# Optimization experiments

Measured on AMD Instinct MI355X. Metric: run time of the kernel, lower is better.

Reference implementation:

```python
import jax, jax.numpy as jnp
import numpy as np

B, C, H, W = 8, 256, 56, 56
R = 2
E = C // R  # embed_dim = in_channels // r


def setup_inputs() -> dict:
    key = jax.random.key(0)
    ks = jax.random.split(key, 10)
    s = 0.02
    return {
        "x": jax.random.normal(ks[0], (B, C, H, W), jnp.float32),
        "Wq": jax.random.normal(ks[1], (E, C), jnp.float32) * s,
        "bq": jax.random.normal(ks[2], (E,), jnp.float32) * s,
        "Wk": jax.random.normal(ks[3], (E, C), jnp.float32) * s,
        "bk": jax.random.normal(ks[4], (E,), jnp.float32) * s,
        "Wv": jax.random.normal(ks[5], (E, C), jnp.float32) * s,
        "bv": jax.random.normal(ks[6], (E,), jnp.float32) * s,
        "Wcat": jax.random.normal(ks[7], (1, 2 * E), jnp.float32) * s,  # 1x1 conv, no bias
        "Wexp": jax.random.normal(ks[8], (C, E), jnp.float32) * s,
        "bexp": jax.random.normal(ks[9], (C,), jnp.float32) * s,
    }


def reference(x, Wq, bq, Wk, bk, Wv, bv, Wcat, Wexp, bexp):
    b, c, h, w = x.shape
    n = h * w
    xf = x.reshape(b, c, n)  # 1x1 convs are channel matmuls over flattened pixels
    q = jnp.einsum('ec,bcn->ben', Wq, xf) + bq[None, :, None]   # [b,E,n]
    k = jnp.einsum('ec,bcn->ben', Wk, xf) + bk[None, :, None]   # [b,E,n]
    v = jnp.einsum('ec,bcn->bne', Wv, xf) + bv[None, None, :]   # [b,n,E]
    # concat_project 1x1 conv on qk=[q;k] repeated along a new n2 axis.
    # NOTE: source repeats BOTH q and k as 'b c n1 -> b c n1 n2', so the score
    # is constant along n2: s[b,n1] = ReLU(wq.q[:,n1] + wk.k[:,n1]).
    wq_c, wk_c = Wcat[0, :E], Wcat[0, E:]
    s = jax.nn.relu(jnp.einsum('e,ben->bn', wq_c, q)
                    + jnp.einsum('e,ben->bn', wk_c, k))         # [b,n]
    attn = jnp.broadcast_to(s[:, :, None], (b, n, n)) / n       # [b,n,n]
    embed = jnp.einsum('bij,bje->bie', attn, v)                 # [b,n,E]
    out = jnp.einsum('ce,bne->bcn', Wexp, embed) + bexp[None, :, None]
    return out.reshape(b, c, h, w) + x
```

## Files before the change

kernel.cpp:

```cpp
#include <hip/hip_runtime.h>

#define CC 256
#define EE 128
#define BB 8
#define NN 3136
#define NN4 784
#define T4 8
#define NTILES 98

__device__ __forceinline__ float waveReduceSum(float v) {
    #pragma unroll
    for (int off = 32; off > 0; off >>= 1) v += __shfl_down(v, off, 64);
    return v;
}

__global__ void __launch_bounds__(256) kA(
        const float* __restrict__ x,
        const float* __restrict__ Wq, const float* __restrict__ bq,
        const float* __restrict__ Wk, const float* __restrict__ bk,
        const float* __restrict__ Wv, const float* __restrict__ bv,
        const float* __restrict__ Wcat, const float* __restrict__ Wexp,
        float* __restrict__ xbar, float* __restrict__ MgT, float* __restrict__ hg,
        float* __restrict__ Ag, float* __restrict__ cst) {
    const int blk = blockIdx.x;
    const int tid = threadIdx.x;
    if (blk == 0) {
        float a = 0.f;
        #pragma unroll 8
        for (int e = 0; e < EE; e++)
            a += Wcat[e] * Wq[e * CC + tid] + Wcat[EE + e] * Wk[e * CC + tid];
        Ag[tid] = a;
        if (tid < 64) {
            float cp = Wcat[tid] * bq[tid] + Wcat[tid + 64] * bq[tid + 64]
                     + Wcat[EE + tid] * bk[tid] + Wcat[EE + tid + 64] * bk[tid + 64];
            cp = waveReduceSum(cp);
            if (tid == 0) cst[0] = cp;
        }
    } else if (blk <= CC) {
        const int r = blk - 1;
        __shared__ float we_s[EE];
        if (tid < EE) we_s[tid] = Wexp[r * EE + tid];
        __syncthreads();
        float m = 0.f;
        #pragma unroll 8
        for (int e = 0; e < EE; e++) m += we_s[e] * Wv[e * CC + tid];
        MgT[tid * CC + r] = m;
        if (tid < 64) {
            float hp = we_s[tid] * bv[tid] + we_s[tid + 64] * bv[tid + 64];
            hp = waveReduceSum(hp);
            if (tid == 0) hg[r] = hp;
        }
    } else {
        const int row = blk - (CC + 1);
        const float4* xr = (const float4*)(x + (size_t)row * NN);
        float acc = 0.f;
        for (int i = tid; i < NN4; i += 256) {
            float4 v = xr[i];
            acc += (v.x + v.y) + (v.z + v.w);
        }
        acc = waveReduceSum(acc);
        __shared__ float red[4];
        int wid = tid >> 6, lane = tid & 63;
        if (lane == 0) red[wid] = acc;
        __syncthreads();
        if (tid == 0) xbar[row] = (red[0] + red[1] + red[2] + red[3]) * (1.0f / NN);
    }
}

__global__ void __launch_bounds__(256, 4) kB(
        const float* __restrict__ x, const float* __restrict__ xbar,
        const float* __restrict__ MgT, const float* __restrict__ hg,
        const float* __restrict__ Ag, const float* __restrict__ cst,
        const float* __restrict__ bexp, float* __restrict__ out) {
    const int b    = blockIdx.x / NTILES;
    const int tile = blockIdx.x - b * NTILES;
    const int tid  = threadIdx.x;
    const int i4l = tid & 7, cgr = tid >> 3;

    __shared__ float A_s[CC];
    __shared__ float xb_s[CC];
    __shared__ float g_s[CC];
    __shared__ float be_s[CC];
    __shared__ float4 part[32][8];
    __shared__ float4 s_s[8];

    A_s[tid]  = Ag[tid];
    xb_s[tid] = xbar[b * CC + tid];
    be_s[tid] = bexp[tid];
    __syncthreads();

    const float4* x4 = (const float4*)x + (size_t)b * CC * NN4 + tile * T4;
    float4*       o4 = (float4*)out     + (size_t)b * CC * NN4 + tile * T4;

    float4 xc[8];
    #pragma unroll
    for (int j = 0; j < 8; j++)
        xc[j] = x4[(size_t)(cgr * 8 + j) * NN4 + i4l];

    float g = hg[tid];
    #pragma unroll 8
    for (int k = 0; k < CC; k++)
        g = fmaf(MgT[k * CC + tid], xb_s[k], g);
    g_s[tid] = g;

    float4 acc4 = make_float4(0.f, 0.f, 0.f, 0.f);
    #pragma unroll
    for (int j = 0; j < 8; j++) {
        const float a = A_s[cgr * 8 + j];
        const float4 v = xc[j];
        acc4.x = fmaf(a, v.x, acc4.x);
        acc4.y = fmaf(a, v.y, acc4.y);
        acc4.z = fmaf(a, v.z, acc4.z);
        acc4.w = fmaf(a, v.w, acc4.w);
    }
    part[cgr][i4l] = acc4;
    __syncthreads();

    if (tid < 8) {
        float4 sum = part[0][tid];
        #pragma unroll
        for (int g2 = 1; g2 < 32; g2++) {
            float4 p = part[g2][tid];
            sum.x += p.x; sum.y += p.y; sum.z += p.z; sum.w += p.w;
        }
        const float cv = cst[0];
        float4 s;
        s.x = fmaxf(sum.x + cv, 0.f);
        s.y = fmaxf(sum.y + cv, 0.f);
        s.z = fmaxf(sum.z + cv, 0.f);
        s.w = fmaxf(sum.w + cv, 0.f);
        s_s[tid] = s;
    }
    __syncthreads();

    const float4 sv = s_s[i4l];
    #pragma unroll
    for (int j = 0; j < 8; j++) {
        const int c = cgr * 8 + j;
        const float gg = g_s[c];
        const float be = be_s[c];
        const float4 xv = xc[j];
        float4 o;
        o.x = fmaf(sv.x, gg, xv.x) + be;
        o.y = fmaf(sv.y, gg, xv.y) + be;
        o.z = fmaf(sv.z, gg, xv.z) + be;
        o.w = fmaf(sv.w, gg, xv.w) + be;
        o4[(size_t)c * NN4 + i4l] = o;
    }
}

extern "C" void kernel_launch(void* const* d_in, const int* in_sizes, int n_in,
                              void* d_out, int out_size, void* d_ws, size_t ws_size,
                              hipStream_t stream) {
    const float* x    = (const float*)d_in[0];
    const float* Wq   = (const float*)d_in[1];
    const float* bq   = (const float*)d_in[2];
    const float* Wk   = (const float*)d_in[3];
    const float* bk   = (const float*)d_in[4];
    const float* Wv   = (const float*)d_in[5];
    const float* bv   = (const float*)d_in[6];
    const float* Wcat = (const float*)d_in[7];
    const float* Wexp = (const float*)d_in[8];
    const float* bexp = (const float*)d_in[9];
    float* out = (float*)d_out;

    float* ws   = (float*)d_ws;
    float* xbar = ws;
    float* Ag   = ws + 2048;
    float* cst  = ws + 2304;
    float* hg   = ws + 2320;
    float* MgT  = ws + 2576;

    kA<<<1 + CC + BB * CC, 256, 0, stream>>>(x, Wq, bq, Wk, bk, Wv, bv, Wcat, Wexp,
                                             xbar, MgT, hg, Ag, cst);
    kB<<<BB * NTILES, 256, 0, stream>>>(x, xbar, MgT, hg, Ag, cst, bexp, out);
}
```

Before: 116.6 us.

## Fuse both kernels into one persistent kernel with a grid-wide atomic barrier

```diff
diff --git a/kernel.cpp b/kernel.cpp
--- a/kernel.cpp
+++ b/kernel.cpp
@@ -7,6 +7,8 @@
 #define NN4 784
 #define T4 8
 #define NTILES 98
+#define GRID 392
+#define SCOPE __HIP_MEMORY_SCOPE_AGENT
 
 __device__ __forceinline__ float waveReduceSum(float v) {
     #pragma unroll
@@ -14,44 +16,45 @@
     return v;
 }
 
-__global__ void __launch_bounds__(256) kA(
+__global__ void __launch_bounds__(256, 4) mega(
         const float* __restrict__ x,
         const float* __restrict__ Wq, const float* __restrict__ bq,
         const float* __restrict__ Wk, const float* __restrict__ bk,
         const float* __restrict__ Wv, const float* __restrict__ bv,
         const float* __restrict__ Wcat, const float* __restrict__ Wexp,
-        float* __restrict__ xbar, float* __restrict__ MgT, float* __restrict__ hg,
-        float* __restrict__ Ag, float* __restrict__ cst) {
-    const int blk = blockIdx.x;
-    const int tid = threadIdx.x;
-    if (blk == 0) {
+        const float* __restrict__ bexp, float* __restrict__ out,
+        float* __restrict__ xbar, float* __restrict__ Ag,
+        float* __restrict__ cstg, unsigned int* __restrict__ cnt)
+{
+    const int blk = blockIdx.x, tid = threadIdx.x;
+    const int wid = tid >> 6, lane = tid & 63;
+
+    __shared__ float red[4];
+    __shared__ float xb_s[CC];
+    __shared__ float u_part[2][EE];
+    __shared__ float u_s[EE];
+    __shared__ float g_s[CC];
+    __shared__ float A_s[CC];
+    __shared__ float be_s[CC];
+    __shared__ float cv_s;
+    __shared__ float4 part[32][8];
+    __shared__ float4 s_s[8];
+
+    if (blk == GRID - 1) {
         float a = 0.f;
         #pragma unroll 8
         for (int e = 0; e < EE; e++)
             a += Wcat[e] * Wq[e * CC + tid] + Wcat[EE + e] * Wk[e * CC + tid];
-        Ag[tid] = a;
+        __hip_atomic_store(&Ag[tid], a, __ATOMIC_RELEASE, SCOPE);
         if (tid < 64) {
             float cp = Wcat[tid] * bq[tid] + Wcat[tid + 64] * bq[tid + 64]
                      + Wcat[EE + tid] * bk[tid] + Wcat[EE + tid + 64] * bk[tid + 64];
             cp = waveReduceSum(cp);
-            if (tid == 0) cst[0] = cp;
-        }
-    } else if (blk <= CC) {
-        const int r = blk - 1;
-        __shared__ float we_s[EE];
-        if (tid < EE) we_s[tid] = Wexp[r * EE + tid];
-        __syncthreads();
-        float m = 0.f;
-        #pragma unroll 8
-        for (int e = 0; e < EE; e++) m += we_s[e] * Wv[e * CC + tid];
-        MgT[tid * CC + r] = m;
-        if (tid < 64) {
-            float hp = we_s[tid] * bv[tid] + we_s[tid + 64] * bv[tid + 64];
-            hp = waveReduceSum(hp);
-            if (tid == 0) hg[r] = hp;
-        }
-    } else {
-        const int row = blk - (CC + 1);
+            if (tid == 0) __hip_atomic_store(&cstg[0], cp, __ATOMIC_RELEASE, SCOPE);
+        }
+    }
+
+    for (int row = blk; row < BB * CC; row += GRID) {
         const float4* xr = (const float4*)(x + (size_t)row * NN);
         float acc = 0.f;
         for (int i = tid; i < NN4; i += 256) {
@@ -59,93 +62,121 @@
             acc += (v.x + v.y) + (v.z + v.w);
         }
         acc = waveReduceSum(acc);
-        __shared__ float red[4];
-        int wid = tid >> 6, lane = tid & 63;
+        __syncthreads();
         if (lane == 0) red[wid] = acc;
         __syncthreads();
-        if (tid == 0) xbar[row] = (red[0] + red[1] + red[2] + red[3]) * (1.0f / NN);
-    }
-}
-
-__global__ void __launch_bounds__(256, 4) kB(
-        const float* __restrict__ x, const float* __restrict__ xbar,
-        const float* __restrict__ MgT, const float* __restrict__ hg,
-        const float* __restrict__ Ag, const float* __restrict__ cst,
-        const float* __restrict__ bexp, float* __restrict__ out) {
-    const int b    = blockIdx.x / NTILES;
-    const int tile = blockIdx.x - b * NTILES;
-    const int tid  = threadIdx.x;
+        if (tid == 0)
+            __hip_atomic_store(&xbar[row],
+                               (red[0] + red[1] + red[2] + red[3]) * (1.0f / NN),
+                               __ATOMIC_RELEASE, SCOPE);
+    }
+
+    __syncthreads();
+    if (tid == 0) {
+        __threadfence();
+        __hip_atomic_fetch_add(cnt, 1u, __ATOMIC_ACQ_REL, SCOPE);
+        while (__hip_atomic_load(cnt, __ATOMIC_ACQUIRE, SCOPE) < (unsigned)GRID)
+            __builtin_amdgcn_s_sleep(2);
+    }
+    __syncthreads();
+
+    const int t0  = blk * 2;
+    const int b   = t0 / NTILES;
+    const int tl0 = t0 - b * NTILES;
+
+    xb_s[tid] = __hip_atomic_load(&xbar[b * CC + tid], __ATOMIC_ACQUIRE, SCOPE);
+    A_s[tid]  = __hip_atomic_load(&Ag[tid], __ATOMIC_ACQUIRE, SCOPE);
+    be_s[tid] = bexp[tid];
+    if (tid == 0) cv_s = __hip_atomic_load(&cstg[0], __ATOMIC_ACQUIRE, SCOPE);
+    __syncthreads();
+
+    {
+        const int e = tid & 127, h = tid >> 7;
+        const float4* wv4 = (const float4*)(Wv + (size_t)e * CC + h * 128);
+        const float* xbh = xb_s + h * 128;
+        float up = 0.f;
+        #pragma unroll
+        for (int i = 0; i < 32; i++) {
+            float4 w = wv4[i];
+            up = fmaf(w.x, xbh[i * 4 + 0], up);
+            up = fmaf(w.y, xbh[i * 4 + 1], up);
+            up = fmaf(w.z, xbh[i * 4 + 2], up);
+            up = fmaf(w.w, xbh[i * 4 + 3], up);
+        }
+        u_part[h][e] = up;
+    }
+    __syncthreads();
+    if (tid < EE) u_s[tid] = u_part[0][tid] + u_part[1][tid] + bv[tid];
+    __syncthreads();
+    {
+        const float4* we4 = (const float4*)(Wexp + (size_t)tid * EE);
+        float g = 0.f;
+        #pragma unroll
+        for (int i = 0; i < 32; i++) {
+            float4 w = we4[i];
+            g = fmaf(w.x, u_s[i * 4 + 0], g);
+            g = fmaf(w.y, u_s[i * 4 + 1], g);
+            g = fmaf(w.z, u_s[i * 4 + 2], g);
+            g = fmaf(w.w, u_s[i * 4 + 3], g);
+        }
+        g_s[tid] = g;
+    }
+    __syncthreads();
+
     const int i4l = tid & 7, cgr = tid >> 3;
-
-    __shared__ float A_s[CC];
-    __shared__ float xb_s[CC];
-    __shared__ float g_s[CC];
-    __shared__ float be_s[CC];
-    __shared__ float4 part[32][8];
-    __shared__ float4 s_s[8];
-
-    A_s[tid]  = Ag[tid];
-    xb_s[tid] = xbar[b * CC + tid];
-    be_s[tid] = bexp[tid];
-    __syncthreads();
-
-    const float4* x4 = (const float4*)x + (size_t)b * CC * NN4 + tile * T4;
-    float4*       o4 = (float4*)out     + (size_t)b * CC * NN4 + tile * T4;
-
-    float4 xc[8];
-    #pragma unroll
-    for (int j = 0; j < 8; j++)
-        xc[j] = x4[(size_t)(cgr * 8 + j) * NN4 + i4l];
-
-    float g = hg[tid];
-    #pragma unroll 8
-    for (int k = 0; k < CC; k++)
-        g = fmaf(MgT[k * CC + tid], xb_s[k], g);
-    g_s[tid] = g;
-
-    float4 acc4 = make_float4(0.f, 0.f, 0.f, 0.f);
-    #pragma unroll
-    for (int j = 0; j < 8; j++) {
-        const float a = A_s[cgr * 8 + j];
-        const float4 v = xc[j];
-        acc4.x = fmaf(a, v.x, acc4.x);
-        acc4.y = fmaf(a, v.y, acc4.y);
-        acc4.z = fmaf(a, v.z, acc4.z);
-        acc4.w = fmaf(a, v.w, acc4.w);
-    }
-    part[cgr][i4l] = acc4;
-    __syncthreads();
-
-    if (tid < 8) {
-        float4 sum = part[0][tid];
-        #pragma unroll
-        for (int g2 = 1; g2 < 32; g2++) {
-            float4 p = part[g2][tid];
-            sum.x += p.x; sum.y += p.y; sum.z += p.z; sum.w += p.w;
-        }
-        const float cv = cst[0];
-        float4 s;
-        s.x = fmaxf(sum.x + cv, 0.f);
-        s.y = fmaxf(sum.y + cv, 0.f);
-        s.z = fmaxf(sum.z + cv, 0.f);
-        s.w = fmaxf(sum.w + cv, 0.f);
-        s_s[tid] = s;
-    }
-    __syncthreads();
-
-    const float4 sv = s_s[i4l];
-    #pragma unroll
-    for (int j = 0; j < 8; j++) {
-        const int c = cgr * 8 + j;
-        const float gg = g_s[c];
-        const float be = be_s[c];
-        const float4 xv = xc[j];
-        float4 o;
-        o.x = fmaf(sv.x, gg, xv.x) + be;
-        o.y = fmaf(sv.y, gg, xv.y) + be;
-        o.z = fmaf(sv.z, gg, xv.z) + be;
-        o.w = fmaf(sv.w, gg, xv.w) + be;
-        o4[(size_t)c * NN4 + i4l] = o;
+    const float4* xb4 = (const float4*)x + (size_t)b * CC * NN4;
+    float4*       ob4 = (float4*)out    + (size_t)b * CC * NN4;
+
+    for (int tt = 0; tt < 2; tt++) {
+        const int tile = tl0 + tt;
+        const float4* x4 = xb4 + tile * T4;
+        float4*       o4 = ob4 + tile * T4;
+
+        float4 xc[8];
+        float4 acc4 = make_float4(0.f, 0.f, 0.f, 0.f);
+        #pragma unroll
+        for (int j = 0; j < 8; j++) {
+            const int c = cgr * 8 + j;
+            float4 v = x4[(size_t)c * NN4 + i4l];
+            xc[j] = v;
+            const float a = A_s[c];
+            acc4.x = fmaf(a, v.x, acc4.x);
+            acc4.y = fmaf(a, v.y, acc4.y);
+            acc4.z = fmaf(a, v.z, acc4.z);
+            acc4.w = fmaf(a, v.w, acc4.w);
+        }
+        part[cgr][i4l] = acc4;
+        __syncthreads();
+        if (tid < 8) {
+            float4 sum = part[0][tid];
+            #pragma unroll
+            for (int g2 = 1; g2 < 32; g2++) {
+                float4 p = part[g2][tid];
+                sum.x += p.x; sum.y += p.y; sum.z += p.z; sum.w += p.w;
+            }
+            const float cv = cv_s;
+            float4 s;
+            s.x = fmaxf(sum.x + cv, 0.f);
+            s.y = fmaxf(sum.y + cv, 0.f);
+            s.z = fmaxf(sum.z + cv, 0.f);
+            s.w = fmaxf(sum.w + cv, 0.f);
+            s_s[tid] = s;
+        }
+        __syncthreads();
+        const float4 sv = s_s[i4l];
+        #pragma unroll
+        for (int j = 0; j < 8; j++) {
+            const int c = cgr * 8 + j;
+            const float g  = g_s[c];
+            const float be = be_s[c];
+            const float4 xv = xc[j];
+            float4 o;
+            o.x = fmaf(sv.x, g, xv.x) + be;
+            o.y = fmaf(sv.y, g, xv.y) + be;
+            o.z = fmaf(sv.z, g, xv.z) + be;
+            o.w = fmaf(sv.w, g, xv.w) + be;
+            o4[(size_t)c * NN4 + i4l] = o;
+        }
     }
 }
 
@@ -167,11 +198,10 @@
     float* ws   = (float*)d_ws;
     float* xbar = ws;
     float* Ag   = ws + 2048;
-    float* cst  = ws + 2304;
-    float* hg   = ws + 2320;
-    float* MgT  = ws + 2576;
-
-    kA<<<1 + CC + BB * CC, 256, 0, stream>>>(x, Wq, bq, Wk, bk, Wv, bv, Wcat, Wexp,
-                                             xbar, MgT, hg, Ag, cst);
-    kB<<<BB * NTILES, 256, 0, stream>>>(x, xbar, MgT, hg, Ag, cst, bexp, out);
+    float* cstg = ws + 2304;
+    unsigned int* cnt = (unsigned int*)(ws + 2320);
+
+    hipMemsetAsync(cnt, 0, sizeof(unsigned int), stream);
+    mega<<<GRID, 256, 0, stream>>>(x, Wq, bq, Wk, bk, Wv, bv, Wcat, Wexp, bexp,
+                                   out, xbar, Ag, cstg, cnt);
 }
```

New measurement: 269.5 us. 131% more time.
